# Kernel tuning notes

Measured on AMD Instinct MI355X. Metric: run time of the kernel, lower is better.

Reference implementation:

```python
import jax, jax.numpy as jnp
import numpy as np

N_HEAD = 16


def setup_inputs() -> dict:
    key = jax.random.key(0)
    ks = jax.random.split(key, 5)
    B, T, C = 4, 2048, 1024
    s = 0.02
    return {
        "x": jax.random.normal(ks[0], (B, T, C), dtype=jnp.float32),
        "Wq": jax.random.normal(ks[1], (C, C), dtype=jnp.float32) * s,
        "Wk": jax.random.normal(ks[2], (C, C), dtype=jnp.float32) * s,
        "Wv": jax.random.normal(ks[3], (C, C), dtype=jnp.float32) * s,
        "Wp": jax.random.normal(ks[4], (C, C), dtype=jnp.float32) * s,
    }


def reference(x, Wq, Wk, Wv, Wp):
    B, T, C = x.shape
    H = N_HEAD
    D = C // H
    # torch Linear(bias=False): x @ W.T
    q = (x @ Wq.T).reshape(B, T, H, D).transpose(0, 2, 1, 3)  # [B,H,T,D]
    k = (x @ Wk.T).reshape(B, T, H, D).transpose(0, 2, 1, 3)
    v = (x @ Wv.T).reshape(B, T, H, D).transpose(0, 2, 1, 3)
    scale = 1.0 / jnp.sqrt(jnp.float32(D))
    att = jnp.einsum("bhqd,bhkd->bhqk", q, k) * scale  # [B,H,T,T]
    causal = jnp.tril(jnp.ones((T, T), dtype=bool))
    att = jnp.where(causal, att, jnp.float32(-jnp.inf))
    att = jax.nn.softmax(att, axis=-1)
    y = jnp.einsum("bhqk,bhkd->bhqd", att, v)  # [B,H,T,D]
    y = y.transpose(0, 2, 1, 3).reshape(B, T, C)
    return y @ Wp.T
```

## Files before the change

kernel.cpp:

```cpp
#include <hip/hip_runtime.h>
#include <hip/hip_bf16.h>
#include <math.h>

typedef __hip_bfloat16 bf16;
typedef __attribute__((ext_vector_type(8))) short short8;
typedef __attribute__((ext_vector_type(4))) float f32x4;
typedef __attribute__((ext_vector_type(2))) unsigned uint2v;
typedef __attribute__((ext_vector_type(4))) unsigned uint4v;

#define MFMA_BF16(a, b, c) __builtin_amdgcn_mfma_f32_16x16x32_bf16((a), (b), (c), 0, 0, 0)

__device__ __forceinline__ void async_copy16(const bf16* g, bf16* l) {
  __builtin_amdgcn_global_load_lds(
      (const __attribute__((address_space(1))) void*)g,
      (__attribute__((address_space(3))) void*)l,
      16, 0, 0);
}

__device__ __forceinline__ unsigned short f2bf_bits(float f) {
  bf16 h = __float2bfloat16(f);
  return *reinterpret_cast<unsigned short*>(&h);
}

__device__ __forceinline__ unsigned cvt_pk_bf16(float lo, float hi) {
  unsigned r;
  asm("v_cvt_pk_bf16_f32 %0, %1, %2" : "=v"(r) : "v"(lo), "v"(hi));
  return r;
}

__global__ __launch_bounds__(256) void cvt_all(const float* __restrict__ x,
                                               const float* __restrict__ wq,
                                               const float* __restrict__ wk,
                                               const float* __restrict__ wv,
                                               const float* __restrict__ wp,
                                               bf16* __restrict__ xb, bf16* __restrict__ wqb,
                                               bf16* __restrict__ wkb, bf16* __restrict__ wvb,
                                               bf16* __restrict__ wpb) {
  const int bid = blockIdx.x;
  const float* in;
  bf16* out;
  int off;
  float scale = 1.0f;
  if (bid < 4096) {
    in = x; out = xb; off = bid;
  } else if (bid < 4608) {
    in = wq; out = wqb; off = bid - 4096;
    scale = 0.180336880111112f;
  } else if (bid < 5120) {
    in = wk; out = wkb; off = bid - 4608;
  } else if (bid < 5632) {
    in = wv; out = wvb; off = bid - 5120;
  } else {
    in = wp; out = wpb; off = bid - 5632;
  }
  const int base = off * 512 + threadIdx.x * 2;
#pragma unroll
  for (int u = 0; u < 2; ++u) {
    const int i = base + u;
    float4 v = reinterpret_cast<const float4*>(in)[i];
    ushort4 pk;
    pk.x = f2bf_bits(v.x * scale);
    pk.y = f2bf_bits(v.y * scale);
    pk.z = f2bf_bits(v.z * scale);
    pk.w = f2bf_bits(v.w * scale);
    reinterpret_cast<ushort4*>(out)[i] = pk;
  }
}

template <int NZ>
__device__ __forceinline__ void gemm_fused_core(const bf16* __restrict__ A,
                                                const bf16* __restrict__ w0,
                                                const bf16* __restrict__ w1,
                                                const bf16* __restrict__ w2,
                                                int bx, int by,
                                                f32x4 (&acc)[NZ][4][4]) {
  __shared__ __align__(16) bf16 L[3][8192 + NZ * 4096];
  const int t = threadIdx.x;
  const int lane = t & 63;
  const int l15 = lane & 15;
  const int quad = (lane >> 4) & 3;
  const int wave = t >> 6;
  const int wm = (wave >> 1) * 64;
  const int wn = (wave & 1) * 64;
  const int K = 1024;

  const f32x4 zero = {0.f, 0.f, 0.f, 0.f};
#pragma unroll
  for (int z = 0; z < NZ; ++z)
#pragma unroll
    for (int m = 0; m < 4; ++m)
#pragma unroll
      for (int n = 0; n < 4; ++n) acc[z][m][n] = zero;

  const int srow = t >> 2;
  const int schunk = ((t & 3) ^ ((t >> 3) & 3)) * 8;
  const bf16* ga0 = A + (size_t)(by * 256 + srow) * K + schunk;
  const bf16* ga1 = ga0 + (size_t)128 * K;
  const bf16* ws[3] = {w0, w1, w2};
  const bf16* gw[NZ];
#pragma unroll
  for (int z = 0; z < NZ; ++z)
    gw[z] = ws[z] + (size_t)(bx * 128 + srow) * K + schunk;

  const int fsw = (quad ^ ((l15 >> 1) & 3)) * 8;
  const int arow = (wm + l15) * 32 + fsw;
  const int brow = (wn + l15) * 32 + fsw;

  auto stage = [&](int kt) {
    bf16* Ld = &L[kt % 3][0];
    async_copy16(ga0 + kt * 32, Ld + t * 8);
    async_copy16(ga1 + kt * 32, Ld + 4096 + t * 8);
#pragma unroll
    for (int z = 0; z < NZ; ++z)
      async_copy16(gw[z] + kt * 32, Ld + 8192 + z * 4096 + t * 8);
  };

  stage(0);
  stage(1);
  if constexpr (NZ == 3)
    asm volatile("s_waitcnt vmcnt(5)" ::: "memory");
  else
    asm volatile("s_waitcnt vmcnt(3)" ::: "memory");
  __builtin_amdgcn_s_barrier();

  for (int T = 0; T < 32; ++T) {
    const bf16* Lb = &L[T % 3][0];
    short8 af[4];
#pragma unroll
    for (int m = 0; m < 4; ++m)
      af[m] = *reinterpret_cast<const short8*>(Lb + arow + m * 512);
    if (T <= 29) {
      stage(T + 2);
      if constexpr (NZ == 3)
        asm volatile("s_waitcnt vmcnt(5)" ::: "memory");
      else
        asm volatile("s_waitcnt vmcnt(3)" ::: "memory");
    } else {
      asm volatile("s_waitcnt vmcnt(0)" ::: "memory");
    }
    __builtin_amdgcn_s_barrier();
    asm volatile("s_waitcnt lgkmcnt(0)" ::: "memory");
    __builtin_amdgcn_sched_barrier(0);
    __builtin_amdgcn_s_setprio(1);
#pragma unroll
    for (int z = 0; z < NZ; ++z) {
      short8 bfr[4];
#pragma unroll
      for (int n = 0; n < 4; ++n)
        bfr[n] = *reinterpret_cast<const short8*>(Lb + 8192 + z * 4096 + brow + n * 512);
#pragma unroll
      for (int m = 0; m < 4; ++m)
#pragma unroll
        for (int n = 0; n < 4; ++n) acc[z][m][n] = MFMA_BF16(af[m], bfr[n], acc[z][m][n]);
    }
    __builtin_amdgcn_s_setprio(0);
    __builtin_amdgcn_sched_barrier(0);
    __builtin_amdgcn_s_barrier();
  }
}

__device__ __forceinline__ void xcd_map(int i, int& bx, int& by) {
  bx = (i >> 3) & 7;
  by = (i & 7) * 4 + (i >> 6);
}

__global__ __launch_bounds__(512, 2) void gemm_qkv(const bf16* __restrict__ x,
                                                   const bf16* __restrict__ wq,
                                                   const bf16* __restrict__ wk,
                                                   const bf16* __restrict__ wv,
                                                   bf16* __restrict__ q, bf16* __restrict__ k,
                                                   bf16* __restrict__ vt) {
  int bx, by;
  xcd_map(blockIdx.x, bx, by);
  f32x4 acc[3][4][4];
  gemm_fused_core<3>(x, wq, wk, wv, bx, by, acc);
  const int t = threadIdx.x, lane = t & 63, l15 = lane & 15, quad = (lane >> 4) & 3,
            wave = t >> 6;
  const int wm = (wave >> 1) * 64, wn = (wave & 1) * 64;
  const int rb = by * 256 + wm + quad * 4;
  const int cbb = bx * 128 + wn + l15;
#pragma unroll
  for (int z = 0; z < 2; ++z) {
    bf16* C = z ? k : q;
#pragma unroll
    for (int m = 0; m < 4; ++m)
#pragma unroll
      for (int n = 0; n < 4; ++n)
#pragma unroll
        for (int r = 0; r < 4; ++r)
          C[(size_t)(rb + m * 16 + r) * 1024 + cbb + n * 16] = __float2bfloat16(acc[z][m][n][r]);
  }
#pragma unroll
  for (int m = 0; m < 4; ++m)
#pragma unroll
    for (int n = 0; n < 4; ++n) {
      const int tg = rb + m * 16;
      const int col = cbb + n * 16;
      const int b = tg >> 11, tl = tg & 2047;
      const int tls = (tl & ~12) | ((tl & 4) << 1) | ((tl & 8) >> 1);
      ushort4 pk;
      pk.x = f2bf_bits(acc[2][m][n][0]);
      pk.y = f2bf_bits(acc[2][m][n][1]);
      pk.z = f2bf_bits(acc[2][m][n][2]);
      pk.w = f2bf_bits(acc[2][m][n][3]);
      *reinterpret_cast<ushort4*>(&vt[((size_t)(b * 1024 + col)) * 2048 + tls]) = pk;
    }
}

__global__ __launch_bounds__(512, 2) void gemm_proj(const bf16* __restrict__ y,
                                                    const bf16* __restrict__ wp,
                                                    float* __restrict__ outp) {
  int bx, by;
  xcd_map(blockIdx.x, bx, by);
  f32x4 acc[1][4][4];
  gemm_fused_core<1>(y, wp, wp, wp, bx, by, acc);
  const int t = threadIdx.x, lane = t & 63, l15 = lane & 15, quad = (lane >> 4) & 3,
            wave = t >> 6;
  const int wm = (wave >> 1) * 64, wn = (wave & 1) * 64;
  const int rb = by * 256 + wm + quad * 4;
  const int cbb = bx * 128 + wn + l15;
#pragma unroll
  for (int m = 0; m < 4; ++m)
#pragma unroll
    for (int n = 0; n < 4; ++n)
#pragma unroll
      for (int r = 0; r < 4; ++r)
        outp[(size_t)(rb + m * 16 + r) * 1024 + cbb + n * 16] = acc[0][m][n][r];
}

__global__ __launch_bounds__(256, 3) void attn(const bf16* __restrict__ qb,
                                               const bf16* __restrict__ kb,
                                               const bf16* __restrict__ vt,
                                               bf16* __restrict__ yb) {
  __shared__ __align__(16) bf16 Ks[2][4096];
  __shared__ __align__(16) bf16 Vs[2][4096];
  const int tid = threadIdx.x;
  const int lane = tid & 63, l15 = lane & 15, quad = lane >> 4, wave = tid >> 6;
  const int p = blockIdx.y;
  const int bh = blockIdx.x;
  const int b = bh >> 4, h = bh & 15;
  const size_t rowbase = (size_t)b * 2048;
  const int cb = h * 64;

  const int tlo = p, thi = 31 - p;
  const int gq0[2] = {tlo * 64 + wave * 16, thi * 64 + wave * 16};

  short8 aq[2][2];
#pragma unroll
  for (int g = 0; g < 2; ++g) {
    const bf16* qp = qb + (rowbase + gq0[g] + l15) * 1024 + cb + quad * 8;
    aq[g][0] = *reinterpret_cast<const short8*>(qp);
    aq[g][1] = *reinterpret_cast<const short8*>(qp + 32);
  }

  short8 ones;
#pragma unroll
  for (int i = 0; i < 8; ++i) ones[i] = (short)0x3F80;

  f32x4 o[2][4], l4[2];
  const f32x4 zero = {0.f, 0.f, 0.f, 0.f};
#pragma unroll
  for (int g = 0; g < 2; ++g) {
#pragma unroll
    for (int dt = 0; dt < 4; ++dt) o[g][dt] = zero;
    l4[g] = zero;
  }

  const int srow = tid >> 3;
  const int sc = (tid & 7) ^ (srow & 7);
  const bf16* kg = kb + (rowbase + srow) * 1024 + cb + sc * 8;
  const bf16* vg = vt + ((size_t)bh * 64 + srow) * 2048 + sc * 8;
  const int fx = l15 & 7;

  const int nkt = thi + 1;
  async_copy16(kg, &Ks[0][tid * 8]);
  async_copy16(kg + 32 * 1024, &Ks[0][2048 + tid * 8]);
  async_copy16(vg, &Vs[0][tid * 8]);
  async_copy16(vg + (size_t)32 * 2048, &Vs[0][2048 + tid * 8]);

  for (int kt = 0; kt < nkt; ++kt) {
    const int buf = kt & 1;
    __syncthreads();
    if (kt + 1 < nkt) {
      const bf16* kgn = kg + (size_t)(kt + 1) * 64 * 1024;
      const bf16* vgn = vg + (kt + 1) * 64;
      async_copy16(kgn, &Ks[buf ^ 1][tid * 8]);
      async_copy16(kgn + 32 * 1024, &Ks[buf ^ 1][2048 + tid * 8]);
      async_copy16(vgn, &Vs[buf ^ 1][tid * 8]);
      async_copy16(vgn + (size_t)32 * 2048, &Vs[buf ^ 1][2048 + tid * 8]);
    }
    const int k0g = kt * 64;

    short8 bk[4][2];
#pragma unroll
    for (int j = 0; j < 4; ++j)
#pragma unroll
      for (int ks = 0; ks < 2; ++ks)
        bk[j][ks] = *reinterpret_cast<const short8*>(
            &Ks[buf][(j * 16 + l15) * 64 + (((ks * 4 + quad) ^ fx)) * 8]);

#pragma unroll
    for (int g = 0; g < 2; ++g) {
      if (k0g > gq0[g] + 15) continue;
      f32x4 st[4];
#pragma unroll
      for (int j = 0; j < 4; ++j) {
        st[j] = MFMA_BF16(bk[j][0], aq[g][0], zero);
        st[j] = MFMA_BF16(bk[j][1], aq[g][1], st[j]);
      }
      const int rem = gq0[g] + 15 - k0g;
      const bool need_mask = (k0g + 63 > gq0[g]);
      unsigned w[4][2] = {{0u, 0u}, {0u, 0u}, {0u, 0u}, {0u, 0u}};
#pragma unroll
      for (int j = 0; j < 4; ++j) {
        if (j * 16 <= rem) {
          float pw[4];
#pragma unroll
          for (int r = 0; r < 4; ++r) {
            float val = st[j][r];
            if (need_mask && (k0g + j * 16 + quad * 4 + r) > (gq0[g] + l15))
              val = -INFINITY;
            pw[r] = __builtin_amdgcn_exp2f(val);
          }
          w[j][0] = cvt_pk_bf16(pw[0], pw[1]);
          w[j][1] = cvt_pk_bf16(pw[2], pw[3]);
        }
      }
#pragma unroll
      for (int half = 0; half < 2; ++half) {
        uint2v s0 =
            __builtin_amdgcn_permlane32_swap(w[2 * half][0], w[2 * half + 1][0], false, false);
        uint2v s1 =
            __builtin_amdgcn_permlane32_swap(w[2 * half][1], w[2 * half + 1][1], false, false);
        uint4v u;
        u[0] = s0[0];
        u[1] = s1[0];
        u[2] = s0[1];
        u[3] = s1[1];
        const short8 bp = __builtin_bit_cast(short8, u);
#pragma unroll
        for (int dt = 0; dt < 4; ++dt) {
          const short8 av = *reinterpret_cast<const short8*>(
              &Vs[buf][(dt * 16 + l15) * 64 + (((half * 4 + quad) ^ fx)) * 8]);
          o[g][dt] = MFMA_BF16(av, bp, o[g][dt]);
        }
        l4[g] = MFMA_BF16(ones, bp, l4[g]);
      }
    }
  }

#pragma unroll
  for (int g = 0; g < 2; ++g) {
    const float invl = 1.f / l4[g][0];
    bf16* yp = yb + (rowbase + gq0[g] + l15) * 1024 + cb + quad * 4;
#pragma unroll
    for (int dt = 0; dt < 4; ++dt) {
      ushort4 pk;
      pk.x = f2bf_bits(o[g][dt][0] * invl);
      pk.y = f2bf_bits(o[g][dt][1] * invl);
      pk.z = f2bf_bits(o[g][dt][2] * invl);
      pk.w = f2bf_bits(o[g][dt][3] * invl);
      *reinterpret_cast<ushort4*>(&yp[dt * 16]) = pk;
    }
  }
}

extern "C" void kernel_launch(void* const* d_in, const int* in_sizes, int n_in,
                              void* d_out, int out_size, void* d_ws, size_t ws_size,
                              hipStream_t stream) {
  const float* x = (const float*)d_in[0];
  const float* Wq = (const float*)d_in[1];
  const float* Wk = (const float*)d_in[2];
  const float* Wv = (const float*)d_in[3];
  const float* Wp = (const float*)d_in[4];
  float* out = (float*)d_out;

  const size_t MB = 1024 * 1024;
  char* ws = (char*)d_ws;
  bf16* xb = (bf16*)(ws);
  bf16* qb = (bf16*)(ws + 16 * MB);
  bf16* kb = (bf16*)(ws + 32 * MB);
  bf16* vtb = (bf16*)(ws + 48 * MB);
  bf16* wqb = (bf16*)(ws + 64 * MB);
  bf16* wkb = (bf16*)(ws + 66 * MB);
  bf16* wvb = (bf16*)(ws + 68 * MB);
  bf16* wpb = (bf16*)(ws + 70 * MB);
  bf16* yb = xb;

  cvt_all<<<6144, 256, 0, stream>>>(x, Wq, Wk, Wv, Wp, xb, wqb, wkb, wvb, wpb);
  gemm_qkv<<<256, 512, 0, stream>>>(xb, wqb, wkb, wvb, qb, kb, vtb);
  attn<<<dim3(64, 16), 256, 0, stream>>>(qb, kb, vtb, yb);
  gemm_proj<<<256, 512, 0, stream>>>(yb, wpb, out);
}
```

Measured before the change: 241.8 us.

## Split attention query tiles across 8 waves instead of looping per wave

The attention block grows from 256 to 512 threads. Each wave now owns one query group: the low or high tile of the balanced causal pair. Before, each wave handled both groups in sequence. K/V staging is spread over twice as many threads, so each thread issues one async copy per tile instead of two. This doubles wave-level parallelism and cuts per-wave register use, in exchange for more waves contending for LDS reads. Waves on the low tile also sit idle at barriers once their causal range is exhausted.

```diff
diff --git a/kernel.cpp b/kernel.cpp
--- a/kernel.cpp
+++ b/kernel.cpp
@@ -228,14 +228,14 @@
         outp[(size_t)(rb + m * 16 + r) * 1024 + cbb + n * 16] = acc[0][m][n][r];
 }
 
-__global__ __launch_bounds__(256, 3) void attn(const bf16* __restrict__ qb,
+__global__ __launch_bounds__(512, 2) void attn(const bf16* __restrict__ qb,
                                                const bf16* __restrict__ kb,
                                                const bf16* __restrict__ vt,
                                                bf16* __restrict__ yb) {
   __shared__ __align__(16) bf16 Ks[2][4096];
   __shared__ __align__(16) bf16 Vs[2][4096];
   const int tid = threadIdx.x;
-  const int lane = tid & 63, l15 = lane & 15, quad = lane >> 4, wave = tid >> 6;
+  const int lane = tid & 63, l15 = lane & 15, quad = (lane >> 4) & 3, wave = tid >> 6;
   const int p = blockIdx.y;
   const int bh = blockIdx.x;
   const int b = bh >> 4, h = bh & 15;
@@ -243,28 +243,27 @@
   const int cb = h * 64;
 
   const int tlo = p, thi = 31 - p;
-  const int gq0[2] = {tlo * 64 + wave * 16, thi * 64 + wave * 16};
-
-  short8 aq[2][2];
-#pragma unroll
-  for (int g = 0; g < 2; ++g) {
-    const bf16* qp = qb + (rowbase + gq0[g] + l15) * 1024 + cb + quad * 8;
-    aq[g][0] = *reinterpret_cast<const short8*>(qp);
-    aq[g][1] = *reinterpret_cast<const short8*>(qp + 32);
+  const int g = wave >> 2;
+  const int w4 = wave & 3;
+  const int qt = g ? thi : tlo;
+  const int gq0 = qt * 64 + w4 * 16;
+
+  short8 aq[2];
+  {
+    const bf16* qp = qb + (rowbase + gq0 + l15) * 1024 + cb + quad * 8;
+    aq[0] = *reinterpret_cast<const short8*>(qp);
+    aq[1] = *reinterpret_cast<const short8*>(qp + 32);
   }
 
   short8 ones;
 #pragma unroll
   for (int i = 0; i < 8; ++i) ones[i] = (short)0x3F80;
 
-  f32x4 o[2][4], l4[2];
+  f32x4 o[4], l4;
   const f32x4 zero = {0.f, 0.f, 0.f, 0.f};
 #pragma unroll
-  for (int g = 0; g < 2; ++g) {
-#pragma unroll
-    for (int dt = 0; dt < 4; ++dt) o[g][dt] = zero;
-    l4[g] = zero;
-  }
+  for (int dt = 0; dt < 4; ++dt) o[dt] = zero;
+  l4 = zero;
 
   const int srow = tid >> 3;
   const int sc = (tid & 7) ^ (srow & 7);
@@ -274,42 +273,34 @@
 
   const int nkt = thi + 1;
   async_copy16(kg, &Ks[0][tid * 8]);
-  async_copy16(kg + 32 * 1024, &Ks[0][2048 + tid * 8]);
   async_copy16(vg, &Vs[0][tid * 8]);
-  async_copy16(vg + (size_t)32 * 2048, &Vs[0][2048 + tid * 8]);
 
   for (int kt = 0; kt < nkt; ++kt) {
     const int buf = kt & 1;
     __syncthreads();
     if (kt + 1 < nkt) {
-      const bf16* kgn = kg + (size_t)(kt + 1) * 64 * 1024;
-      const bf16* vgn = vg + (kt + 1) * 64;
-      async_copy16(kgn, &Ks[buf ^ 1][tid * 8]);
-      async_copy16(kgn + 32 * 1024, &Ks[buf ^ 1][2048 + tid * 8]);
-      async_copy16(vgn, &Vs[buf ^ 1][tid * 8]);
-      async_copy16(vgn + (size_t)32 * 2048, &Vs[buf ^ 1][2048 + tid * 8]);
+      async_copy16(kg + (size_t)(kt + 1) * 64 * 1024, &Ks[buf ^ 1][tid * 8]);
+      async_copy16(vg + (kt + 1) * 64, &Vs[buf ^ 1][tid * 8]);
     }
     const int k0g = kt * 64;
 
-    short8 bk[4][2];
-#pragma unroll
-    for (int j = 0; j < 4; ++j)
-#pragma unroll
-      for (int ks = 0; ks < 2; ++ks)
-        bk[j][ks] = *reinterpret_cast<const short8*>(
-            &Ks[buf][(j * 16 + l15) * 64 + (((ks * 4 + quad) ^ fx)) * 8]);
-
-#pragma unroll
-    for (int g = 0; g < 2; ++g) {
-      if (k0g > gq0[g] + 15) continue;
+    if (k0g <= gq0 + 15) {
+      short8 bk[4][2];
+#pragma unroll
+      for (int j = 0; j < 4; ++j)
+#pragma unroll
+        for (int ks = 0; ks < 2; ++ks)
+          bk[j][ks] = *reinterpret_cast<const short8*>(
+              &Ks[buf][(j * 16 + l15) * 64 + (((ks * 4 + quad) ^ fx)) * 8]);
+
       f32x4 st[4];
 #pragma unroll
       for (int j = 0; j < 4; ++j) {
-        st[j] = MFMA_BF16(bk[j][0], aq[g][0], zero);
-        st[j] = MFMA_BF16(bk[j][1], aq[g][1], st[j]);
+        st[j] = MFMA_BF16(bk[j][0], aq[0], zero);
+        st[j] = MFMA_BF16(bk[j][1], aq[1], st[j]);
       }
-      const int rem = gq0[g] + 15 - k0g;
-      const bool need_mask = (k0g + 63 > gq0[g]);
+      const int rem = gq0 + 15 - k0g;
+      const bool need_mask = (k0g + 63 > gq0);
       unsigned w[4][2] = {{0u, 0u}, {0u, 0u}, {0u, 0u}, {0u, 0u}};
 #pragma unroll
       for (int j = 0; j < 4; ++j) {
@@ -318,7 +309,7 @@
 #pragma unroll
           for (int r = 0; r < 4; ++r) {
             float val = st[j][r];
-            if (need_mask && (k0g + j * 16 + quad * 4 + r) > (gq0[g] + l15))
+            if (need_mask && (k0g + j * 16 + quad * 4 + r) > (gq0 + l15))
               val = -INFINITY;
             pw[r] = __builtin_amdgcn_exp2f(val);
           }
@@ -342,24 +333,23 @@
         for (int dt = 0; dt < 4; ++dt) {
           const short8 av = *reinterpret_cast<const short8*>(
               &Vs[buf][(dt * 16 + l15) * 64 + (((half * 4 + quad) ^ fx)) * 8]);
-          o[g][dt] = MFMA_BF16(av, bp, o[g][dt]);
+          o[dt] = MFMA_BF16(av, bp, o[dt]);
         }
-        l4[g] = MFMA_BF16(ones, bp, l4[g]);
+        l4 = MFMA_BF16(ones, bp, l4);
       }
     }
   }
 
-#pragma unroll
-  for (int g = 0; g < 2; ++g) {
-    const float invl = 1.f / l4[g][0];
-    bf16* yp = yb + (rowbase + gq0[g] + l15) * 1024 + cb + quad * 4;
+  {
+    const float invl = 1.f / l4[0];
+    bf16* yp = yb + (rowbase + gq0 + l15) * 1024 + cb + quad * 4;
 #pragma unroll
     for (int dt = 0; dt < 4; ++dt) {
       ushort4 pk;
-      pk.x = f2bf_bits(o[g][dt][0] * invl);
-      pk.y = f2bf_bits(o[g][dt][1] * invl);
-      pk.z = f2bf_bits(o[g][dt][2] * invl);
-      pk.w = f2bf_bits(o[g][dt][3] * invl);
+      pk.x = f2bf_bits(o[dt][0] * invl);
+      pk.y = f2bf_bits(o[dt][1] * invl);
+      pk.z = f2bf_bits(o[dt][2] * invl);
+      pk.w = f2bf_bits(o[dt][3] * invl);
       *reinterpret_cast<ushort4*>(&yp[dt * 16]) = pk;
     }
   }
@@ -389,6 +379,6 @@
 
   cvt_all<<<6144, 256, 0, stream>>>(x, Wq, Wk, Wv, Wp, xb, wqb, wkb, wvb, wpb);
   gemm_qkv<<<256, 512, 0, stream>>>(xb, wqb, wkb, wvb, qb, kb, vtb);
-  attn<<<dim3(64, 16), 256, 0, stream>>>(qb, kb, vtb, yb);
+  attn<<<dim3(64, 16), 512, 0, stream>>>(qb, kb, vtb, yb);
   gemm_proj<<<256, 512, 0, stream>>>(yb, wpb, out);
 }
```

New measurement: 232.7 us. -3.7%, faster.
